# Kernel tuning notes

Hardware: AMD Instinct MI355X
Metric: run time of the kernel (lower is better)

Reference implementation:

```python
import jax, jax.numpy as jnp
import numpy as np

N_DOMAIN = 10
DOM_EMB = 4
IN_DIM = 1024
HIDDEN = [1024, 512, 256]
N_EXPERTS = 8
LORA_R = 16


def _glorot(key, shape):
    fan_in, fan_out = shape[-2], shape[-1]
    lim = np.sqrt(6.0 / (fan_in + fan_out))
    return jax.random.uniform(key, shape, jnp.float32, -lim, lim)


def setup_inputs() -> dict:
    key = jax.random.key(0)
    ks = jax.random.split(key, 32)
    inp = {
        "dnn_input": jax.random.normal(ks[0], (16384, IN_DIM), jnp.float32),
        "domain_input": jax.random.randint(ks[1], (16384,), 0, N_DOMAIN, jnp.int64),
        "emb_table": jax.random.normal(ks[2], (N_DOMAIN, DOM_EMB), jnp.float32),
        "gate_W": _glorot(ks[3], (DOM_EMB, N_EXPERTS)),
        "gate_b": jnp.zeros((N_EXPERTS,), jnp.float32),
    }
    prev = IN_DIM
    k = 4
    for li, h in enumerate(HIDDEN):
        inp[f"W{li}"] = _glorot(ks[k], (prev, h)); k += 1
        inp[f"b{li}"] = jnp.zeros((h,), jnp.float32)
        # original inits B and lora_bias to zeros; use small randoms so outputs/grads are non-trivial
        inp[f"A{li}"] = _glorot(ks[k], (N_EXPERTS, prev, LORA_R)); k += 1
        inp[f"B{li}"] = 0.01 * jax.random.normal(ks[k], (N_EXPERTS, LORA_R, h), jnp.float32); k += 1
        inp[f"lb{li}"] = 0.01 * jax.random.normal(ks[k], (N_EXPERTS, h), jnp.float32); k += 1
        prev = h
    return inp


def _moe_layer(x, gate, W, b, A, B, lb):
    # base GEMM (dropout is identity: rate 0 / inference)
    base = x @ W + b                                   # [B, h]
    t = jnp.einsum('bp,epr->ber', x, A)                # [B, E, r]
    eo = jnp.einsum('ber,erh->beh', t, B) + lb[None]   # [B, E, h]
    moe = jnp.einsum('be,beh->bh', gate, eo)           # [B, h]
    return jax.nn.relu(base + moe)


def reference(dnn_input, domain_input, emb_table, gate_W, gate_b,
              W0, b0, A0, B0, lb0,
              W1, b1, A1, B1, lb1,
              W2, b2, A2, B2, lb2):
    dom = emb_table[domain_input]                      # [B, 4]
    gate = jax.nn.softmax(dom @ gate_W + gate_b, axis=-1)  # [B, E]
    x = dnn_input
    x = _moe_layer(x, gate, W0, b0, A0, B0, lb0)
    x = _moe_layer(x, gate, W1, b1, A1, B1, lb1)
    x = _moe_layer(x, gate, W2, b2, A2, B2, lb2)
    return x
```

## Files before the change

### kernel.cpp

```cpp
#include <hip/hip_runtime.h>
#include <hip/hip_bf16.h>
#include <stdint.h>

#define KAUG 192
#define M_ROWS 16384

typedef __attribute__((ext_vector_type(8))) __bf16 bf16x8;
typedef __attribute__((ext_vector_type(4))) float f32x4;

__device__ __forceinline__ unsigned short f2b(float f) {
  unsigned int u = __builtin_bit_cast(unsigned int, f);
  u = (u + 0x7fffu + ((u >> 16) & 1u)) >> 16;
  return (unsigned short)u;
}

__device__ __forceinline__ void lds_load16(const unsigned short* g, unsigned short* l) {
  __builtin_amdgcn_global_load_lds(
      (const __attribute__((address_space(1))) void*)g,
      (__attribute__((address_space(3))) void*)l, 16, 0, 0);
}

template<int N> __device__ __forceinline__ void vmcnt_wait() {
  if constexpr (N == 0)      asm volatile("s_waitcnt vmcnt(0)" ::: "memory");
  else if constexpr (N == 3) asm volatile("s_waitcnt vmcnt(3)" ::: "memory");
  else if constexpr (N == 4) asm volatile("s_waitcnt vmcnt(4)" ::: "memory");
  else if constexpr (N == 6) asm volatile("s_waitcnt vmcnt(6)" ::: "memory");
  else                       asm volatile("s_waitcnt vmcnt(8)" ::: "memory");
}


__global__ void gate_kernel(const int* __restrict__ dom, const float* __restrict__ emb,
                            const float* __restrict__ gW, const float* __restrict__ gb,
                            float* __restrict__ gate) {
  int i = blockIdx.x * blockDim.x + threadIdx.x;
  int d = dom[i];
  float e0 = emb[d*4+0], e1 = emb[d*4+1], e2 = emb[d*4+2], e3 = emb[d*4+3];
  float l[8]; float mx = -1e30f;
#pragma unroll
  for (int j = 0; j < 8; j++) {
    l[j] = e0*gW[j] + e1*gW[8+j] + e2*gW[16+j] + e3*gW[24+j] + gb[j];
    mx = fmaxf(mx, l[j]);
  }
  float s = 0.f;
#pragma unroll
  for (int j = 0; j < 8; j++) { l[j] = __expf(l[j] - mx); s += l[j]; }
  float inv = 1.0f / s;
#pragma unroll
  for (int j = 0; j < 8; j++) gate[i*8+j] = l[j] * inv;
}

__global__ void f32_to_bf16_vec(const float* __restrict__ in, unsigned short* __restrict__ out, int n4) {
  int i = blockIdx.x * blockDim.x + threadIdx.x;
  if (i >= n4) return;
  float4 v = ((const float4*)in)[i];
  ushort4 o;
  o.x = f2b(v.x); o.y = f2b(v.y); o.z = f2b(v.z); o.w = f2b(v.w);
  ((ushort4*)out)[i] = o;
}

__global__ void build_wt_t(const float* __restrict__ W, unsigned short* __restrict__ Wt,
                           int K, int N) {
  __shared__ float tl[32][33];
  int n0 = blockIdx.x * 32, k0 = blockIdx.y * 32;
  int tx = threadIdx.x & 31, ty = threadIdx.x >> 5;
#pragma unroll
  for (int i = 0; i < 32; i += 8)
    tl[ty + i][tx] = W[(long)(k0 + ty + i) * N + n0 + tx];
  __syncthreads();
#pragma unroll
  for (int i = 0; i < 32; i += 8)
    Wt[(long)(n0 + ty + i) * K + k0 + tx] = f2b(tl[tx][ty + i]);
}

__global__ void build_aft_t(const float* __restrict__ A, unsigned short* __restrict__ Aft, int P) {
  __shared__ float tl[64][17];
  int e = blockIdx.y; long p0 = (long)blockIdx.x * 64;
  int t = threadIdx.x;
#pragma unroll
  for (int pass = 0; pass < 4; pass++) {
    int idx = t + pass * 256;
    int pl = idx >> 4, r = idx & 15;
    tl[pl][r] = A[((long)e * P + p0 + pl) * 16 + r];
  }
  __syncthreads();
#pragma unroll
  for (int pass = 0; pass < 4; pass++) {
    int idx = t + pass * 256;
    int r = idx >> 6, pl = idx & 63;
    Aft[(long)(e * 16 + r) * P + p0 + pl] = f2b(tl[pl][r]);
  }
}

__global__ void build_bft_t(const float* __restrict__ Bm, const float* __restrict__ lb,
                            unsigned short* __restrict__ Bft, int H) {
  __shared__ float tl[32][33];
  int n0 = blockIdx.x * 32, kk0 = blockIdx.y * 32;
  int tx = threadIdx.x & 31, ty = threadIdx.x >> 5;
#pragma unroll
  for (int i = 0; i < 32; i += 8) {
    int kk = kk0 + ty + i;
    float v;
    if (kk < 128)       v = Bm[(long)kk * H + n0 + tx];
    else if (kk < 136)  v = lb[(long)(kk - 128) * H + n0 + tx];
    else                v = 0.f;
    tl[ty + i][tx] = v;
  }
  __syncthreads();
#pragma unroll
  for (int i = 0; i < 32; i += 8)
    Bft[(long)(n0 + ty + i) * KAUG + kk0 + tx] = f2b(tl[tx][ty + i]);
}

__global__ void aug_fill(const float* __restrict__ gate, unsigned short* __restrict__ tg) {
  int i = blockIdx.x * blockDim.x + threadIdx.x;
  int j = i & 63; int b = i >> 6;
  float v = (j < 8) ? gate[b*8 + j] : 0.f;
  tg[(long)b * KAUG + 128 + j] = f2b(v);
}

template<int MODE, int BM>
__global__ __launch_bounds__(512)
void gemm_mn(const unsigned short* __restrict__ A1, int lda1, int K1,
             const unsigned short* __restrict__ A2, int lda2, int K2,
             const unsigned short* __restrict__ Bt1, int ldb1,
             const unsigned short* __restrict__ Bt2, int ldb2,
             const float* __restrict__ bias,
             const float* __restrict__ gate,
             void* __restrict__ outp, int ldout) {
  constexpr int MFRAG = BM / 32;
  constexpr int ATOT = BM * 64;
  constexpr int BTOT = 128 * 64;
  constexpr int LA = BM / 64;
  constexpr int L = LA + 2;
  __shared__ __attribute__((aligned(16))) unsigned short lds[3 * ATOT + 3 * BTOT];

  const int t = threadIdx.x;
  const int lane = t & 63, wave = t >> 6;
  const int wr = wave >> 2, wc = wave & 3;
  const int rl = lane & 15, kg = lane >> 4;
  const int row0 = blockIdx.x * BM, col0 = blockIdx.y * 128;

  const int sr = t >> 3;
  const int sk = ((t & 7) ^ (sr & 7)) * 8;

  f32x4 acc[MFRAG][2];
#pragma unroll
  for (int m = 0; m < MFRAG; m++)
#pragma unroll
    for (int n = 0; n < 2; n++) acc[m][n] = (f32x4){0.f, 0.f, 0.f, 0.f};

  auto stageA = [&](int buf, int kt) {
    const unsigned short* src; long ld; int kl;
    if (kt < K1) { src = A1; ld = lda1; kl = kt; }
    else         { src = A2; ld = lda2; kl = kt - K1; }
    unsigned short* d = &lds[buf * ATOT + t * 8];
    const unsigned short* s = src + (long)(row0 + sr) * ld + kl + sk;
#pragma unroll
    for (int i = 0; i < LA; i++)
      lds_load16(s + (long)(i * 64) * ld, d + i * 4096);
  };
  auto stageB = [&](int buf, int kt) {
    const unsigned short* src; long ld; int kl;
    if (kt < K1) { src = Bt1; ld = ldb1; kl = kt; }
    else         { src = Bt2; ld = ldb2; kl = kt - K1; }
    unsigned short* d = &lds[3 * ATOT + buf * BTOT + t * 8];
    const unsigned short* s = src + (long)(col0 + sr) * ld + kl + sk;
    lds_load16(s, d);
    lds_load16(s + 64 * ld, d + 4096);
  };
  auto ldA = [&](int buf, int mg, int ks) {
    int lr = wr * (BM / 2) + mg * 16 + rl;
    int sc = (ks * 4 + kg) ^ (lr & 7);
    return *(const bf16x8*)&lds[buf * ATOT + lr * 64 + sc * 8];
  };
  auto ldB = [&](int buf, int n, int ks) {
    int cr = wc * 32 + n * 16 + rl;
    int sc = (ks * 4 + kg) ^ (cr & 7);
    return *(const bf16x8*)&lds[3 * ATOT + buf * BTOT + cr * 64 + sc * 8];
  };

  const int Ktot = K1 + K2;
  const int NT = Ktot / 64;

  stageA(0, 0); stageB(0, 0);
  stageA(1, 64); stageB(1, 64);
  vmcnt_wait<L>();
  __builtin_amdgcn_s_barrier();

  int bcur = 0;
  bf16x8 Bfv[2][2];
  for (int tt = 0; tt < NT; ++tt) {
    int bpf = bcur + 2; if (bpf > 2) bpf -= 3;
    const bool pf = (tt + 2 < NT);
    bf16x8 Af[(MFRAG + 1) / 2][2];
#pragma unroll
    for (int m = 0; m < MFRAG / 2; m++) { Af[m][0] = ldA(bcur, m, 0); Af[m][1] = ldA(bcur, m, 1); }
#pragma unroll
    for (int n = 0; n < 2; n++) { Bfv[n][0] = ldB(bcur, n, 0); Bfv[n][1] = ldB(bcur, n, 1); }
    if (pf) stageA(bpf, (tt + 2) * 64);
    __builtin_amdgcn_s_barrier();
    asm volatile("s_waitcnt lgkmcnt(0)" ::: "memory");
    __builtin_amdgcn_sched_barrier(0);
    __builtin_amdgcn_s_setprio(1);
#pragma unroll
    for (int m = 0; m < MFRAG / 2; m++)
#pragma unroll
      for (int n = 0; n < 2; n++) {
        acc[m][n] = __builtin_amdgcn_mfma_f32_16x16x32_bf16(Af[m][0], Bfv[n][0], acc[m][n], 0, 0, 0);
        acc[m][n] = __builtin_amdgcn_mfma_f32_16x16x32_bf16(Af[m][1], Bfv[n][1], acc[m][n], 0, 0, 0);
      }
    __builtin_amdgcn_s_setprio(0);
    __builtin_amdgcn_s_barrier();
#pragma unroll
    for (int m = 0; m < MFRAG / 2; m++) { Af[m][0] = ldA(bcur, MFRAG / 2 + m, 0); Af[m][1] = ldA(bcur, MFRAG / 2 + m, 1); }
    if (pf) stageB(bpf, (tt + 2) * 64);
    if (tt + 1 < NT) vmcnt_wait<L>();
    else             vmcnt_wait<0>();
    __builtin_amdgcn_s_barrier();
    asm volatile("s_waitcnt lgkmcnt(0)" ::: "memory");
    __builtin_amdgcn_sched_barrier(0);
    __builtin_amdgcn_s_setprio(1);
#pragma unroll
    for (int m = 0; m < MFRAG / 2; m++)
#pragma unroll
      for (int n = 0; n < 2; n++) {
        acc[MFRAG / 2 + m][n] = __builtin_amdgcn_mfma_f32_16x16x32_bf16(Af[m][0], Bfv[n][0], acc[MFRAG / 2 + m][n], 0, 0, 0);
        acc[MFRAG / 2 + m][n] = __builtin_amdgcn_mfma_f32_16x16x32_bf16(Af[m][1], Bfv[n][1], acc[MFRAG / 2 + m][n], 0, 0, 0);
      }
    __builtin_amdgcn_s_setprio(0);
    __builtin_amdgcn_s_barrier();
    bcur = bcur == 2 ? 0 : bcur + 1;
  }

#pragma unroll
  for (int m = 0; m < MFRAG; m++)
#pragma unroll
    for (int n = 0; n < 2; n++)
#pragma unroll
      for (int j = 0; j < 4; j++) {
        int row = row0 + wr * (BM / 2) + m * 16 + kg * 4 + j;
        int col = col0 + wc * 32 + n * 16 + rl;
        float v = acc[m][n][j];
        if (MODE == 0) {
          v *= gate[row * 8 + (col >> 4)];
          ((unsigned short*)outp)[(long)row * ldout + col] = f2b(v);
        } else {
          v += bias[col];
          v = fmaxf(v, 0.f);
          if (MODE == 1) ((unsigned short*)outp)[(long)row * ldout + col] = f2b(v);
          else           ((float*)outp)[(long)row * ldout + col] = v;
        }
      }
}

template<int MODE>
__global__ __launch_bounds__(256, 2)
void gemm_w128(const unsigned short* __restrict__ A1, int lda1, int K1,
               const unsigned short* __restrict__ A2, int lda2, int K2,
               const unsigned short* __restrict__ Bt1, int ldb1,
               const unsigned short* __restrict__ Bt2, int ldb2,
               const float* __restrict__ bias,
               void* __restrict__ outp, int ldout) {
  constexpr int ATOT = 256 * 32;
  constexpr int BTOT = 128 * 32;
  __shared__ __attribute__((aligned(16))) unsigned short lds[2 * ATOT + 2 * BTOT];

  const int t = threadIdx.x;
  const int lane = t & 63, wave = t >> 6;
  const int wr = wave >> 1, wc = wave & 1;
  const int rl = lane & 15, kg = lane >> 4;
  const int row0 = blockIdx.x * 256, col0 = blockIdx.y * 128;

  const int sr = t >> 2;
  const int sk = ((t & 3) ^ ((sr >> 1) & 3)) * 8;

  f32x4 acc[8][4];
#pragma unroll
  for (int m = 0; m < 8; m++)
#pragma unroll
    for (int n = 0; n < 4; n++) acc[m][n] = (f32x4){0.f, 0.f, 0.f, 0.f};

  auto stageA = [&](int buf, int kt) {
    const unsigned short* src; long ld; int kl;
    if (kt < K1) { src = A1; ld = lda1; kl = kt; }
    else         { src = A2; ld = lda2; kl = kt - K1; }
    unsigned short* d = &lds[buf * ATOT + t * 8];
    const unsigned short* s = src + (long)(row0 + sr) * ld + kl + sk;
#pragma unroll
    for (int i = 0; i < 4; i++)
      lds_load16(s + (long)(i * 64) * ld, d + i * 2048);
  };
  auto stageB = [&](int buf, int kt) {
    const unsigned short* src; long ld; int kl;
    if (kt < K1) { src = Bt1; ld = ldb1; kl = kt; }
    else         { src = Bt2; ld = ldb2; kl = kt - K1; }
    unsigned short* d = &lds[2 * ATOT + buf * BTOT + t * 8];
    const unsigned short* s = src + (long)(col0 + sr) * ld + kl + sk;
    lds_load16(s, d);
    lds_load16(s + 64 * ld, d + 2048);
  };
  auto ldA = [&](int buf, int mf) {
    int lr = wr * 128 + mf * 16 + rl;
    int sc = kg ^ ((lr >> 1) & 3);
    return *(const bf16x8*)&lds[buf * ATOT + lr * 32 + sc * 8];
  };
  auto ldB = [&](int buf, int nf) {
    int cr = wc * 64 + nf * 16 + rl;
    int sc = kg ^ ((cr >> 1) & 3);
    return *(const bf16x8*)&lds[2 * ATOT + buf * BTOT + cr * 32 + sc * 8];
  };

  const int NT = (K1 + K2) / 32;

  stageA(0, 0); stageB(0, 0);
  __syncthreads();

  int cur = 0;
  for (int tt = 0; tt < NT; ++tt) {
    if (tt + 1 < NT) { stageA(cur ^ 1, (tt + 1) * 32); stageB(cur ^ 1, (tt + 1) * 32); }
    bf16x8 Af[8], Bf[4];
#pragma unroll
    for (int nf = 0; nf < 4; nf++) Bf[nf] = ldB(cur, nf);
#pragma unroll
    for (int mf = 0; mf < 8; mf++) Af[mf] = ldA(cur, mf);
#pragma unroll
    for (int mf = 0; mf < 8; mf++)
#pragma unroll
      for (int nf = 0; nf < 4; nf++)
        acc[mf][nf] = __builtin_amdgcn_mfma_f32_16x16x32_bf16(Af[mf], Bf[nf], acc[mf][nf], 0, 0, 0);
    __syncthreads();
    cur ^= 1;
  }

#pragma unroll
  for (int m = 0; m < 8; m++)
#pragma unroll
    for (int n = 0; n < 4; n++)
#pragma unroll
      for (int j = 0; j < 4; j++) {
        int row = row0 + wr * 128 + m * 16 + kg * 4 + j;
        int col = col0 + wc * 64 + n * 16 + rl;
        float v = acc[m][n][j] + bias[col];
        v = fmaxf(v, 0.f);
        if (MODE == 1) ((unsigned short*)outp)[(long)row * ldout + col] = f2b(v);
        else           ((float*)outp)[(long)row * ldout + col] = v;
      }
}


extern "C" void kernel_launch(void* const* d_in, const int* in_sizes, int n_in,
                              void* d_out, int out_size, void* d_ws, size_t ws_size,
                              hipStream_t stream) {
  (void)in_sizes; (void)n_in; (void)out_size; (void)ws_size;
  const float* dnn = (const float*)d_in[0];
  const int*   dom = (const int*)d_in[1];
  const float* emb = (const float*)d_in[2];
  const float* gW  = (const float*)d_in[3];
  const float* gb  = (const float*)d_in[4];
  const float* Wm[3]  = {(const float*)d_in[5],  (const float*)d_in[10], (const float*)d_in[15]};
  const float* bm[3]  = {(const float*)d_in[6],  (const float*)d_in[11], (const float*)d_in[16]};
  const float* Am[3]  = {(const float*)d_in[7],  (const float*)d_in[12], (const float*)d_in[17]};
  const float* Bm[3]  = {(const float*)d_in[8],  (const float*)d_in[13], (const float*)d_in[18]};
  const float* lbm[3] = {(const float*)d_in[9],  (const float*)d_in[14], (const float*)d_in[19]};

  const int M = M_ROWS;
  const int dIn[3]  = {1024, 1024, 512};
  const int dOutN[3] = {1024, 512, 256};

  char* p = (char*)d_ws;
  auto carve = [&](size_t bytes) { char* r = p; p += (bytes + 255) & ~(size_t)255; return r; };
  float* gate = (float*)carve((size_t)M * 8 * sizeof(float));
  unsigned short* xb0 = (unsigned short*)carve((size_t)M * 1024 * 2);
  unsigned short* xb1 = (unsigned short*)carve((size_t)M * 1024 * 2);
  unsigned short* tg  = (unsigned short*)carve((size_t)M * KAUG * 2);
  unsigned short *Wt[3], *Aft[3], *Bft[3];
  for (int l = 0; l < 3; l++) {
    Wt[l]  = (unsigned short*)carve((size_t)dOutN[l] * dIn[l] * 2);
    Aft[l] = (unsigned short*)carve((size_t)128 * dIn[l] * 2);
    Bft[l] = (unsigned short*)carve((size_t)dOutN[l] * KAUG * 2);
  }

  gate_kernel<<<M / 256, 256, 0, stream>>>(dom, emb, gW, gb, gate);
  {
    int n4 = M * 1024 / 4;
    f32_to_bf16_vec<<<(n4 + 255) / 256, 256, 0, stream>>>(dnn, xb0, n4);
  }
  for (int l = 0; l < 3; l++) {
    build_wt_t<<<dim3(dOutN[l] / 32, dIn[l] / 32), 256, 0, stream>>>(Wm[l], Wt[l], dIn[l], dOutN[l]);
    build_aft_t<<<dim3(dIn[l] / 64, 8), 256, 0, stream>>>(Am[l], Aft[l], dIn[l]);
    build_bft_t<<<dim3(dOutN[l] / 32, KAUG / 32), 256, 0, stream>>>(Bm[l], lbm[l], Bft[l], dOutN[l]);
  }
  aug_fill<<<(M * 64) / 256, 256, 0, stream>>>(gate, tg);

  const unsigned short* xin = xb0;
  for (int l = 0; l < 3; l++) {
    int K1 = dIn[l], N = dOutN[l];
    gemm_mn<0, 64><<<dim3(M / 64, 1), 512, 0, stream>>>(
        xin, K1, K1, nullptr, 0, 0, Aft[l], K1, nullptr, 0, nullptr, gate, (void*)tg, KAUG);
    if (l == 0)
      gemm_w128<1><<<dim3(M / 256, N / 128), 256, 0, stream>>>(
          xin, K1, K1, tg, KAUG, KAUG, Wt[l], K1, Bft[l], KAUG, bm[l], (void*)xb1, N);
    else if (l == 1)
      gemm_mn<1, 256><<<dim3(M / 256, N / 128), 512, 0, stream>>>(
          xin, K1, K1, tg, KAUG, KAUG, Wt[l], K1, Bft[l], KAUG, bm[l], nullptr, (void*)xb0, N);
    else
      gemm_mn<2, 128><<<dim3(M / 128, N / 128), 512, 0, stream>>>(
          xin, K1, K1, tg, KAUG, KAUG, Wt[l], K1, Bft[l], KAUG, bm[l], nullptr, d_out, N);
    xin = (l == 0) ? xb1 : xb0;
  }
}
```

Baseline: 162.2 us.

## Replace main GEMMs with BK64 double-buffered kernel and batch prep launches

Replaces the layer GEMMs with a new templated kernel. It uses a 64-wide K tile, 8-way XOR-swizzled LDS, split MFMA phases with setprio and explicit waitcnt/barrier, and smaller M tiles (128/128/64) that allow more blocks per CU. It also merges the per-layer weight-transpose kernels into single launches indexed by blockIdx.z, folds aug_fill into the gate kernel, and widens the input cast to 8 elements per thread. The aim is less launch overhead and better MFMA/LDS overlap and occupancy, at the cost of lower per-block data reuse from the smaller tiles.

```diff
diff --git a/kernel.cpp b/kernel.cpp
--- a/kernel.cpp
+++ b/kernel.cpp
@@ -29,9 +29,9 @@
 }
 
 
-__global__ void gate_kernel(const int* __restrict__ dom, const float* __restrict__ emb,
-                            const float* __restrict__ gW, const float* __restrict__ gb,
-                            float* __restrict__ gate) {
+__global__ void gate_aug_kernel(const int* __restrict__ dom, const float* __restrict__ emb,
+                                const float* __restrict__ gW, const float* __restrict__ gb,
+                                float* __restrict__ gate, unsigned short* __restrict__ tg) {
   int i = blockIdx.x * blockDim.x + threadIdx.x;
   int d = dom[i];
   float e0 = emb[d*4+0], e1 = emb[d*4+1], e2 = emb[d*4+2], e3 = emb[d*4+3];
@@ -45,23 +45,46 @@
 #pragma unroll
   for (int j = 0; j < 8; j++) { l[j] = __expf(l[j] - mx); s += l[j]; }
   float inv = 1.0f / s;
-#pragma unroll
-  for (int j = 0; j < 8; j++) gate[i*8+j] = l[j] * inv;
-}
-
-__global__ void f32_to_bf16_vec(const float* __restrict__ in, unsigned short* __restrict__ out, int n4) {
-  int i = blockIdx.x * blockDim.x + threadIdx.x;
-  if (i >= n4) return;
-  float4 v = ((const float4*)in)[i];
-  ushort4 o;
-  o.x = f2b(v.x); o.y = f2b(v.y); o.z = f2b(v.z); o.w = f2b(v.w);
-  ((ushort4*)out)[i] = o;
-}
-
-__global__ void build_wt_t(const float* __restrict__ W, unsigned short* __restrict__ Wt,
-                           int K, int N) {
+  unsigned int g[4];
+#pragma unroll
+  for (int j = 0; j < 8; j++) {
+    float v = l[j] * inv;
+    gate[i*8+j] = v;
+    unsigned int b = f2b(v);
+    if (j & 1) g[j >> 1] |= b << 16; else g[j >> 1] = b;
+  }
+  uint4* dst = (uint4*)&tg[(long)i * KAUG + 128];
+  dst[0] = make_uint4(g[0], g[1], g[2], g[3]);
+  uint4 z4 = make_uint4(0, 0, 0, 0);
+#pragma unroll
+  for (int q = 1; q < 8; q++) dst[q] = z4;
+}
+
+__global__ void f32_to_bf16_vec(const float* __restrict__ in, unsigned int* __restrict__ out, long n8) {
+  long i = (long)blockIdx.x * blockDim.x + threadIdx.x;
+  if (i >= n8) return;
+  float4 a = ((const float4*)in)[i * 2];
+  float4 b = ((const float4*)in)[i * 2 + 1];
+  uint4 o;
+  o.x = f2b(a.x) | ((unsigned)f2b(a.y) << 16);
+  o.y = f2b(a.z) | ((unsigned)f2b(a.w) << 16);
+  o.z = f2b(b.x) | ((unsigned)f2b(b.y) << 16);
+  o.w = f2b(b.z) | ((unsigned)f2b(b.w) << 16);
+  ((uint4*)out)[i] = o;
+}
+
+__global__ void build_wt_all(const float* __restrict__ w0, const float* __restrict__ w1,
+                             const float* __restrict__ w2,
+                             unsigned short* __restrict__ t0, unsigned short* __restrict__ t1,
+                             unsigned short* __restrict__ t2) {
+  int z = blockIdx.z;
+  const float* W = z == 0 ? w0 : (z == 1 ? w1 : w2);
+  unsigned short* Wt = z == 0 ? t0 : (z == 1 ? t1 : t2);
+  int K = (z == 2) ? 512 : 1024;
+  int N = (z == 0) ? 1024 : (z == 1 ? 512 : 256);
+  int n0 = blockIdx.x * 32, k0 = blockIdx.y * 32;
+  if (n0 >= N || k0 >= K) return;
   __shared__ float tl[32][33];
-  int n0 = blockIdx.x * 32, k0 = blockIdx.y * 32;
   int tx = threadIdx.x & 31, ty = threadIdx.x >> 5;
 #pragma unroll
   for (int i = 0; i < 32; i += 8)
@@ -72,9 +95,18 @@
     Wt[(long)(n0 + ty + i) * K + k0 + tx] = f2b(tl[tx][ty + i]);
 }
 
-__global__ void build_aft_t(const float* __restrict__ A, unsigned short* __restrict__ Aft, int P) {
+__global__ void build_aft_all(const float* __restrict__ a0, const float* __restrict__ a1,
+                              const float* __restrict__ a2,
+                              unsigned short* __restrict__ t0, unsigned short* __restrict__ t1,
+                              unsigned short* __restrict__ t2) {
+  int z = blockIdx.z;
+  const float* A = z == 0 ? a0 : (z == 1 ? a1 : a2);
+  unsigned short* Aft = z == 0 ? t0 : (z == 1 ? t1 : t2);
+  int P = (z == 2) ? 512 : 1024;
+  long p0 = (long)blockIdx.x * 64;
+  if (p0 >= P) return;
+  int e = blockIdx.y;
   __shared__ float tl[64][17];
-  int e = blockIdx.y; long p0 = (long)blockIdx.x * 64;
   int t = threadIdx.x;
 #pragma unroll
   for (int pass = 0; pass < 4; pass++) {
@@ -91,10 +123,20 @@
   }
 }
 
-__global__ void build_bft_t(const float* __restrict__ Bm, const float* __restrict__ lb,
-                            unsigned short* __restrict__ Bft, int H) {
+__global__ void build_bft_all(const float* __restrict__ b0, const float* __restrict__ b1,
+                              const float* __restrict__ b2,
+                              const float* __restrict__ l0, const float* __restrict__ l1,
+                              const float* __restrict__ l2,
+                              unsigned short* __restrict__ t0, unsigned short* __restrict__ t1,
+                              unsigned short* __restrict__ t2) {
+  int z = blockIdx.z;
+  const float* Bm = z == 0 ? b0 : (z == 1 ? b1 : b2);
+  const float* lb = z == 0 ? l0 : (z == 1 ? l1 : l2);
+  unsigned short* Bft = z == 0 ? t0 : (z == 1 ? t1 : t2);
+  int H = (z == 0) ? 1024 : (z == 1 ? 512 : 256);
+  int n0 = blockIdx.x * 32, kk0 = blockIdx.y * 32;
+  if (n0 >= H) return;
   __shared__ float tl[32][33];
-  int n0 = blockIdx.x * 32, kk0 = blockIdx.y * 32;
   int tx = threadIdx.x & 31, ty = threadIdx.x >> 5;
 #pragma unroll
   for (int i = 0; i < 32; i += 8) {
@@ -109,13 +151,6 @@
 #pragma unroll
   for (int i = 0; i < 32; i += 8)
     Bft[(long)(n0 + ty + i) * KAUG + kk0 + tx] = f2b(tl[tx][ty + i]);
-}
-
-__global__ void aug_fill(const float* __restrict__ gate, unsigned short* __restrict__ tg) {
-  int i = blockIdx.x * blockDim.x + threadIdx.x;
-  int j = i & 63; int b = i >> 6;
-  float v = (j < 8) ? gate[b*8 + j] : 0.f;
-  tg[(long)b * KAUG + 128 + j] = f2b(v);
 }
 
 template<int MODE, int BM>
@@ -253,30 +288,33 @@
       }
 }
 
-template<int MODE>
-__global__ __launch_bounds__(256, 2)
-void gemm_w128(const unsigned short* __restrict__ A1, int lda1, int K1,
-               const unsigned short* __restrict__ A2, int lda2, int K2,
-               const unsigned short* __restrict__ Bt1, int ldb1,
-               const unsigned short* __restrict__ Bt2, int ldb2,
-               const float* __restrict__ bias,
-               void* __restrict__ outp, int ldout) {
-  constexpr int ATOT = 256 * 32;
-  constexpr int BTOT = 128 * 32;
+template<int MODE, int BM>
+__global__ __launch_bounds__(256, 4)
+void gemm2b(const unsigned short* __restrict__ A1, int lda1, int K1,
+            const unsigned short* __restrict__ A2, int lda2, int K2,
+            const unsigned short* __restrict__ Bt1, int ldb1,
+            const unsigned short* __restrict__ Bt2, int ldb2,
+            const float* __restrict__ bias,
+            const float* __restrict__ gate,
+            void* __restrict__ outp, int ldout) {
+  constexpr int ATOT = BM * 64;
+  constexpr int BTOT = 128 * 64;
+  constexpr int MF = BM / 64;
+  constexpr int LA = BM / 32;
   __shared__ __attribute__((aligned(16))) unsigned short lds[2 * ATOT + 2 * BTOT];
 
   const int t = threadIdx.x;
   const int lane = t & 63, wave = t >> 6;
   const int wr = wave >> 1, wc = wave & 1;
   const int rl = lane & 15, kg = lane >> 4;
-  const int row0 = blockIdx.x * 256, col0 = blockIdx.y * 128;
-
-  const int sr = t >> 2;
-  const int sk = ((t & 3) ^ ((sr >> 1) & 3)) * 8;
-
-  f32x4 acc[8][4];
-#pragma unroll
-  for (int m = 0; m < 8; m++)
+  const int row0 = blockIdx.x * BM, col0 = blockIdx.y * 128;
+
+  const int sr = t >> 3;
+  const int sk = ((t & 7) ^ (sr & 7)) * 8;
+
+  f32x4 acc[2 * MF][4];
+#pragma unroll
+  for (int m = 0; m < 2 * MF; m++)
 #pragma unroll
     for (int n = 0; n < 4; n++) acc[m][n] = (f32x4){0.f, 0.f, 0.f, 0.f};
 
@@ -287,8 +325,8 @@
     unsigned short* d = &lds[buf * ATOT + t * 8];
     const unsigned short* s = src + (long)(row0 + sr) * ld + kl + sk;
 #pragma unroll
-    for (int i = 0; i < 4; i++)
-      lds_load16(s + (long)(i * 64) * ld, d + i * 2048);
+    for (int i = 0; i < LA; i++)
+      lds_load16(s + (long)(i * 32) * ld, d + i * 2048);
   };
   auto stageB = [&](int buf, int kt) {
     const unsigned short* src; long ld; int kl;
@@ -296,54 +334,84 @@
     else         { src = Bt2; ld = ldb2; kl = kt - K1; }
     unsigned short* d = &lds[2 * ATOT + buf * BTOT + t * 8];
     const unsigned short* s = src + (long)(col0 + sr) * ld + kl + sk;
-    lds_load16(s, d);
-    lds_load16(s + 64 * ld, d + 2048);
-  };
-  auto ldA = [&](int buf, int mf) {
-    int lr = wr * 128 + mf * 16 + rl;
-    int sc = kg ^ ((lr >> 1) & 3);
-    return *(const bf16x8*)&lds[buf * ATOT + lr * 32 + sc * 8];
-  };
-  auto ldB = [&](int buf, int nf) {
+#pragma unroll
+    for (int i = 0; i < 4; i++)
+      lds_load16(s + (long)(i * 32) * ld, d + i * 2048);
+  };
+  auto ldA = [&](int buf, int mf, int ks) {
+    int lr = wr * (BM / 2) + mf * 16 + rl;
+    int sc = (ks * 4 + kg) ^ (lr & 7);
+    return *(const bf16x8*)&lds[buf * ATOT + lr * 64 + sc * 8];
+  };
+  auto ldB = [&](int buf, int nf, int ks) {
     int cr = wc * 64 + nf * 16 + rl;
-    int sc = kg ^ ((cr >> 1) & 3);
-    return *(const bf16x8*)&lds[2 * ATOT + buf * BTOT + cr * 32 + sc * 8];
-  };
-
-  const int NT = (K1 + K2) / 32;
+    int sc = (ks * 4 + kg) ^ (cr & 7);
+    return *(const bf16x8*)&lds[2 * ATOT + buf * BTOT + cr * 64 + sc * 8];
+  };
+
+  const int NT = (K1 + K2) / 64;
 
   stageA(0, 0); stageB(0, 0);
-  __syncthreads();
+  asm volatile("s_waitcnt vmcnt(0)" ::: "memory");
+  __builtin_amdgcn_s_barrier();
 
   int cur = 0;
   for (int tt = 0; tt < NT; ++tt) {
-    if (tt + 1 < NT) { stageA(cur ^ 1, (tt + 1) * 32); stageB(cur ^ 1, (tt + 1) * 32); }
-    bf16x8 Af[8], Bf[4];
-#pragma unroll
-    for (int nf = 0; nf < 4; nf++) Bf[nf] = ldB(cur, nf);
-#pragma unroll
-    for (int mf = 0; mf < 8; mf++) Af[mf] = ldA(cur, mf);
-#pragma unroll
-    for (int mf = 0; mf < 8; mf++)
-#pragma unroll
-      for (int nf = 0; nf < 4; nf++)
-        acc[mf][nf] = __builtin_amdgcn_mfma_f32_16x16x32_bf16(Af[mf], Bf[nf], acc[mf][nf], 0, 0, 0);
-    __syncthreads();
+    const bool pf = (tt + 1 < NT);
+    const int kt1 = (tt + 1) * 64;
+    if (pf) { stageA(cur ^ 1, kt1); stageB(cur ^ 1, kt1); }
+    bf16x8 Am_[MF][2], Bf[4][2];
+#pragma unroll
+    for (int mf = 0; mf < MF; mf++) { Am_[mf][0] = ldA(cur, mf, 0); Am_[mf][1] = ldA(cur, mf, 1); }
+#pragma unroll
+    for (int nf = 0; nf < 4; nf++) { Bf[nf][0] = ldB(cur, nf, 0); Bf[nf][1] = ldB(cur, nf, 1); }
+    asm volatile("s_waitcnt lgkmcnt(0)" ::: "memory");
+    __builtin_amdgcn_sched_barrier(0);
+    __builtin_amdgcn_s_setprio(1);
+#pragma unroll
+    for (int mf = 0; mf < MF; mf++)
+#pragma unroll
+      for (int nf = 0; nf < 4; nf++) {
+        acc[mf][nf] = __builtin_amdgcn_mfma_f32_16x16x32_bf16(Am_[mf][0], Bf[nf][0], acc[mf][nf], 0, 0, 0);
+        acc[mf][nf] = __builtin_amdgcn_mfma_f32_16x16x32_bf16(Am_[mf][1], Bf[nf][1], acc[mf][nf], 0, 0, 0);
+      }
+    __builtin_amdgcn_s_setprio(0);
+#pragma unroll
+    for (int mf = 0; mf < MF; mf++) { Am_[mf][0] = ldA(cur, MF + mf, 0); Am_[mf][1] = ldA(cur, MF + mf, 1); }
+    asm volatile("s_waitcnt lgkmcnt(0)" ::: "memory");
+    __builtin_amdgcn_sched_barrier(0);
+    __builtin_amdgcn_s_setprio(1);
+#pragma unroll
+    for (int mf = 0; mf < MF; mf++)
+#pragma unroll
+      for (int nf = 0; nf < 4; nf++) {
+        acc[MF + mf][nf] = __builtin_amdgcn_mfma_f32_16x16x32_bf16(Am_[mf][0], Bf[nf][0], acc[MF + mf][nf], 0, 0, 0);
+        acc[MF + mf][nf] = __builtin_amdgcn_mfma_f32_16x16x32_bf16(Am_[mf][1], Bf[nf][1], acc[MF + mf][nf], 0, 0, 0);
+      }
+    __builtin_amdgcn_s_setprio(0);
+    if (pf) asm volatile("s_waitcnt vmcnt(0)" ::: "memory");
+    __builtin_amdgcn_s_barrier();
     cur ^= 1;
   }
 
 #pragma unroll
-  for (int m = 0; m < 8; m++)
+  for (int m = 0; m < 2 * MF; m++)
 #pragma unroll
     for (int n = 0; n < 4; n++)
 #pragma unroll
       for (int j = 0; j < 4; j++) {
-        int row = row0 + wr * 128 + m * 16 + kg * 4 + j;
+        int row = row0 + wr * (BM / 2) + m * 16 + kg * 4 + j;
         int col = col0 + wc * 64 + n * 16 + rl;
-        float v = acc[m][n][j] + bias[col];
-        v = fmaxf(v, 0.f);
-        if (MODE == 1) ((unsigned short*)outp)[(long)row * ldout + col] = f2b(v);
-        else           ((float*)outp)[(long)row * ldout + col] = v;
+        float v = acc[m][n][j];
+        if (MODE == 0) {
+          v *= gate[row * 8 + (col >> 4)];
+          ((unsigned short*)outp)[(long)row * ldout + col] = f2b(v);
+        } else {
+          v += bias[col];
+          v = fmaxf(v, 0.f);
+          if (MODE == 1) ((unsigned short*)outp)[(long)row * ldout + col] = f2b(v);
+          else           ((float*)outp)[(long)row * ldout + col] = v;
+        }
       }
 }
 
@@ -380,17 +448,16 @@
     Bft[l] = (unsigned short*)carve((size_t)dOutN[l] * KAUG * 2);
   }
 
-  gate_kernel<<<M / 256, 256, 0, stream>>>(dom, emb, gW, gb, gate);
+  gate_aug_kernel<<<M / 256, 256, 0, stream>>>(dom, emb, gW, gb, gate, tg);
   {
-    int n4 = M * 1024 / 4;
-    f32_to_bf16_vec<<<(n4 + 255) / 256, 256, 0, stream>>>(dnn, xb0, n4);
-  }
-  for (int l = 0; l < 3; l++) {
-    build_wt_t<<<dim3(dOutN[l] / 32, dIn[l] / 32), 256, 0, stream>>>(Wm[l], Wt[l], dIn[l], dOutN[l]);
-    build_aft_t<<<dim3(dIn[l] / 64, 8), 256, 0, stream>>>(Am[l], Aft[l], dIn[l]);
-    build_bft_t<<<dim3(dOutN[l] / 32, KAUG / 32), 256, 0, stream>>>(Bm[l], lbm[l], Bft[l], dOutN[l]);
-  }
-  aug_fill<<<(M * 64) / 256, 256, 0, stream>>>(gate, tg);
+    long n8 = (long)M * 1024 / 8;
+    f32_to_bf16_vec<<<(int)((n8 + 255) / 256), 256, 0, stream>>>(dnn, (unsigned int*)xb0, n8);
+  }
+  build_wt_all<<<dim3(32, 32, 3), 256, 0, stream>>>(Wm[0], Wm[1], Wm[2], Wt[0], Wt[1], Wt[2]);
+  build_aft_all<<<dim3(16, 8, 3), 256, 0, stream>>>(Am[0], Am[1], Am[2], Aft[0], Aft[1], Aft[2]);
+  build_bft_all<<<dim3(32, KAUG / 32, 3), 256, 0, stream>>>(Bm[0], Bm[1], Bm[2],
+                                                            lbm[0], lbm[1], lbm[2],
+                                                            Bft[0], Bft[1], Bft[2]);
 
   const unsigned short* xin = xb0;
   for (int l = 0; l < 3; l++) {
@@ -398,13 +465,13 @@
     gemm_mn<0, 64><<<dim3(M / 64, 1), 512, 0, stream>>>(
         xin, K1, K1, nullptr, 0, 0, Aft[l], K1, nullptr, 0, nullptr, gate, (void*)tg, KAUG);
     if (l == 0)
-      gemm_w128<1><<<dim3(M / 256, N / 128), 256, 0, stream>>>(
-          xin, K1, K1, tg, KAUG, KAUG, Wt[l], K1, Bft[l], KAUG, bm[l], (void*)xb1, N);
+      gemm2b<1, 128><<<dim3(M / 128, N / 128), 256, 0, stream>>>(
+          xin, K1, K1, tg, KAUG, KAUG, Wt[l], K1, Bft[l], KAUG, bm[l], nullptr, (void*)xb1, N);
     else if (l == 1)
-      gemm_mn<1, 256><<<dim3(M / 256, N / 128), 512, 0, stream>>>(
+      gemm2b<1, 128><<<dim3(M / 128, N / 128), 256, 0, stream>>>(
           xin, K1, K1, tg, KAUG, KAUG, Wt[l], K1, Bft[l], KAUG, bm[l], nullptr, (void*)xb0, N);
     else
-      gemm_mn<2, 128><<<dim3(M / 128, N / 128), 512, 0, stream>>>(
+      gemm2b<2, 64><<<dim3(M / 64, N / 128), 256, 0, stream>>>(
           xin, K1, K1, tg, KAUG, KAUG, Wt[l], K1, Bft[l], KAUG, bm[l], nullptr, d_out, N);
     xin = (l == 0) ? xb1 : xb0;
   }
```

New measurement: 139.7 us (median of 3 runs). -13.9%, faster.
